# Optimization experiments

Hardware: AMD Instinct MI355X
Metric: run time of the kernel (lower is better)

## Reference

```python
import jax, jax.numpy as jnp
import numpy as np

LATENT = 256
SELEN = 64
MSIZE = 8
BS = 32
T = 2048
TOUCH_IN = 3
GAZE_IN = 4


def setup_inputs() -> dict:
    key = jax.random.key(0)
    ks = jax.random.split(key, 16)
    kH = 1.0 / np.sqrt(LATENT)

    def u(k, shape):
        return jax.random.uniform(k, shape, jnp.float32, -kH, kH)

    return {
        "touch_d": jax.random.normal(ks[0], (BS, T, TOUCH_IN), jnp.float32),
        "gaze_d": jax.random.normal(ks[1], (BS, T, GAZE_IN), jnp.float32),
        # scale so start + SELEN <= T always (avoids the random fallback branch)
        "l": jax.random.uniform(ks[2], (BS, MSIZE), jnp.float32) * ((T - SELEN) / T),
        "tW_ih": u(ks[3], (4 * LATENT, TOUCH_IN)),
        "tW_hh": u(ks[4], (4 * LATENT, LATENT)),
        "tb_ih": u(ks[5], (4 * LATENT,)),
        "tb_hh": u(ks[6], (4 * LATENT,)),
        "gW_ih": u(ks[7], (4 * LATENT, GAZE_IN)),
        "gW_hh": u(ks[8], (4 * LATENT, LATENT)),
        "gb_ih": u(ks[9], (4 * LATENT,)),
        "gb_hh": u(ks[10], (4 * LATENT,)),
        "t_lin_w": u(ks[11], (LATENT, LATENT)),
        "t_lin_b": u(ks[12], (LATENT,)),
        "g_lin_w": u(ks[13], (LATENT, LATENT)),
        "g_lin_b": u(ks[14], (LATENT,)),
    }


def lstm(x, W_ih, W_hh, b_ih, b_hh):
    # x: [B, T, D] -> outputs [B, T, H]; PyTorch gate order i, f, g, o
    B = x.shape[0]
    H = W_hh.shape[1]
    x_proj = x @ W_ih.T + (b_ih + b_hh)  # [B, T, 4H] precomputed input GEMM

    def step(carry, xt):
        h, c = carry
        gates = xt + h @ W_hh.T
        i, f, g, o = jnp.split(gates, 4, axis=-1)
        c = jax.nn.sigmoid(f) * c + jax.nn.sigmoid(i) * jnp.tanh(g)
        h = jax.nn.sigmoid(o) * jnp.tanh(c)
        return (h, c), h

    h0 = jnp.zeros((B, H), x.dtype)
    _, ys = jax.lax.scan(step, (h0, h0), jnp.swapaxes(x_proj, 0, 1))
    return jnp.swapaxes(ys, 0, 1)


def glimpse_mean(emb, starts):
    # emb: [B, T, H]; starts: [B, M] int window starts; mean over M windows of SELEN
    idx = (starts[:, :, None] + jnp.arange(SELEN)).reshape(emb.shape[0], MSIZE * SELEN)
    gathered = jnp.take_along_axis(emb, idx[..., None], axis=1)  # [B, M*SELEN, H]
    return gathered.mean(axis=1)


def reference(touch_d, gaze_d, l, tW_ih, tW_hh, tb_ih, tb_hh,
              gW_ih, gW_hh, gb_ih, gb_hh, t_lin_w, t_lin_b, g_lin_w, g_lin_b):
    touch_out = lstm(touch_d, tW_ih, tW_hh, tb_ih, tb_hh)
    gaze_out = lstm(gaze_d, gW_ih, gW_hh, gb_ih, gb_hh)
    touch_emb = jax.nn.relu(touch_out) @ t_lin_w.T + t_lin_b  # [B, T, H]
    gaze_emb = jax.nn.relu(gaze_out) @ g_lin_w.T + g_lin_b

    touch_mean = touch_emb.mean(axis=1)
    gaze_mean = gaze_emb.mean(axis=1)

    starts = (l * T).astype(jnp.int32)  # [B, M], guaranteed start + SELEN <= T
    touch_attn = glimpse_mean(touch_emb, starts)
    gaze_attn = glimpse_mean(gaze_emb, starts)

    return jnp.concatenate([touch_mean, touch_attn, gaze_mean, gaze_attn], axis=-1)
```

## Files before the change

### kernel.cpp

```cpp
#include <hip/hip_runtime.h>

#define HDIM 256
#define TLEN 2048
#define SELEN 64
#define MSZ 8

typedef _Float16 f16x2 __attribute__((ext_vector_type(2)));
typedef unsigned int u32x16 __attribute__((ext_vector_type(16)));

__device__ __forceinline__ float dot2f(unsigned int w, unsigned int h, float acc) {
  return __builtin_amdgcn_fdot2(__builtin_bit_cast(f16x2, w),
                                __builtin_bit_cast(f16x2, h), acc, false);
}

__device__ __forceinline__ unsigned int pack2(float a, float b) {
  f16x2 v;
  v.x = (_Float16)a; v.y = (_Float16)b;
  return __builtin_bit_cast(unsigned int, v);
}

__device__ __forceinline__ float sigm(float x)   { return 1.0f / (1.0f + __expf(-x)); }
__device__ __forceinline__ float tanh_f(float x) { return 1.0f - 2.0f / (__expf(2.0f * x) + 1.0f); }

#define WO_OFF    0
#define WIH_OFF   131072
#define CNT_OFF   147456
#define H2_OFF    149504
#define LDS_BYTES 150528

extern __shared__ unsigned char smem[];

#define LOADG16(V, RP, B) do {                                                  \
    float2 a0 = (RP)[(B)+0],  a1 = (RP)[(B)+1],  a2 = (RP)[(B)+2],  a3 = (RP)[(B)+3];   \
    float2 a4 = (RP)[(B)+4],  a5 = (RP)[(B)+5],  a6 = (RP)[(B)+6],  a7 = (RP)[(B)+7];   \
    float2 a8 = (RP)[(B)+8],  a9 = (RP)[(B)+9],  aA = (RP)[(B)+10], aB = (RP)[(B)+11];  \
    float2 aC = (RP)[(B)+12], aD = (RP)[(B)+13], aE = (RP)[(B)+14], aF = (RP)[(B)+15];  \
    V[0]  = pack2(a0.x, a0.y); V[1]  = pack2(a1.x, a1.y);                       \
    V[2]  = pack2(a2.x, a2.y); V[3]  = pack2(a3.x, a3.y);                       \
    V[4]  = pack2(a4.x, a4.y); V[5]  = pack2(a5.x, a5.y);                       \
    V[6]  = pack2(a6.x, a6.y); V[7]  = pack2(a7.x, a7.y);                       \
    V[8]  = pack2(a8.x, a8.y); V[9]  = pack2(a9.x, a9.y);                       \
    V[10] = pack2(aA.x, aA.y); V[11] = pack2(aB.x, aB.y);                       \
    V[12] = pack2(aC.x, aC.y); V[13] = pack2(aD.x, aD.y);                       \
    V[14] = pack2(aE.x, aE.y); V[15] = pack2(aF.x, aF.y);                       \
    __builtin_amdgcn_sched_barrier(0);                                          \
  } while (0)

#define JBLK(WIv, WFv, WGv, Q, HC, OC, PF, JN)                                  \
  { const uint4 hh = HC, wo = OC;                                               \
    if (PF) { HC = hv4[JN]; OC = wo4r[(JN) * 512]; }                            \
    ai = dot2f(WIv[4*(Q)+0], hh.x, ai); af = dot2f(WFv[4*(Q)+0], hh.x, af);     \
    ag = dot2f(WGv[4*(Q)+0], hh.x, ag); ao = dot2f(wo.x,         hh.x, ao);     \
    ai = dot2f(WIv[4*(Q)+1], hh.y, ai); af = dot2f(WFv[4*(Q)+1], hh.y, af);     \
    ag = dot2f(WGv[4*(Q)+1], hh.y, ag); ao = dot2f(wo.y,         hh.y, ao);     \
    ai = dot2f(WIv[4*(Q)+2], hh.z, ai); af = dot2f(WFv[4*(Q)+2], hh.z, af);     \
    ag = dot2f(WGv[4*(Q)+2], hh.z, ag); ao = dot2f(wo.z,         hh.z, ao);     \
    ai = dot2f(WIv[4*(Q)+3], hh.w, ai); af = dot2f(WFv[4*(Q)+3], hh.w, af);     \
    ag = dot2f(WGv[4*(Q)+3], hh.w, ag); ao = dot2f(wo.w,         hh.w, ao);     \
    __builtin_amdgcn_sched_barrier(0); }

__global__ void
__attribute__((amdgpu_flat_work_group_size(512, 512),
               amdgpu_waves_per_eu(2, 2),
               amdgpu_num_vgpr(256)))
lstm_seq_kernel(const float* __restrict__ touch, const float* __restrict__ gaze,
                const float* __restrict__ l,
                const float* __restrict__ tWih, const float* __restrict__ tWhh,
                const float* __restrict__ tbih, const float* __restrict__ tbhh,
                const float* __restrict__ gWih, const float* __restrict__ gWhh,
                const float* __restrict__ gbih, const float* __restrict__ gbhh,
                float* __restrict__ ws)
{
  const int bid  = (int)blockIdx.x;
  const int lsel = bid >> 5;
  const int b    = bid & 31;
  const int tid  = (int)threadIdx.x;
  const int lane = tid & 63;
  const int wv   = tid >> 6;
  const int n    = wv * 32 + (lane & 31);
  const int kh   = lane >> 5;
  const int c0   = kh * 128;

  const float* __restrict__ x   = lsel ? gaze : touch;
  const float* __restrict__ Wih = lsel ? gWih : tWih;
  const float* __restrict__ Whh = lsel ? gWhh : tWhh;
  const float* __restrict__ bih = lsel ? gbih : tbih;
  const float* __restrict__ bhh = lsel ? gbhh : tbhh;
  const int D = lsel ? 4 : 3;

  unsigned int*  woL  = (unsigned int*)(smem + WO_OFF);
  float4*        wihF = (float4*)(smem + WIH_OFF);
  unsigned char* cntL = smem + CNT_OFF;

  u32x16 wi0, wi1, wi2, wi3, wf0, wf1, wf2, wf3, wg0, wg1, wg2, wg3;
  {
    const float2* ri = (const float2*)(Whh + (size_t)n * HDIM + c0);
    const float2* rf = (const float2*)(Whh + (size_t)(n + 256) * HDIM + c0);
    const float2* rg = (const float2*)(Whh + (size_t)(n + 512) * HDIM + c0);
    LOADG16(wi0, ri, 0);  LOADG16(wi1, ri, 16);  LOADG16(wi2, ri, 32);  LOADG16(wi3, ri, 48);
    LOADG16(wf0, rf, 0);  LOADG16(wf1, rf, 16);  LOADG16(wf2, rf, 32);  LOADG16(wf3, rf, 48);
    LOADG16(wg0, rg, 0);  LOADG16(wg1, rg, 16);  LOADG16(wg2, rg, 32);  LOADG16(wg3, rg, 48);
  }
  {
    const float2* ro = (const float2*)(Whh + (size_t)(n + 768) * HDIM + c0);
    uint4* wo4 = (uint4*)woL;
    #pragma unroll
    for (int jb = 0; jb < 4; ++jb) {
      #pragma unroll
      for (int q = 0; q < 4; ++q) {
        const int j = jb * 4 + q;
        float2 e0 = ro[4*j], e1 = ro[4*j+1], e2 = ro[4*j+2], e3 = ro[4*j+3];
        uint4 v;
        v.x = pack2(e0.x, e0.y); v.y = pack2(e1.x, e1.y);
        v.z = pack2(e2.x, e2.y); v.w = pack2(e3.x, e3.y);
        wo4[j * 512 + tid] = v;
      }
      __builtin_amdgcn_sched_barrier(0);
    }
  }

  for (int r = tid; r < 1024; r += 512) {
    const float* wr = Wih + (size_t)r * D;
    float4 v;
    v.x = wr[0]; v.y = wr[1]; v.z = wr[2];
    v.w = (D == 4) ? wr[3] : 0.0f;
    wihF[r] = v;
  }
  __builtin_amdgcn_sched_barrier(0);

  {
    int s0 = (int)(l[b * MSZ + 0] * 2048.0f), s1 = (int)(l[b * MSZ + 1] * 2048.0f);
    int s2 = (int)(l[b * MSZ + 2] * 2048.0f), s3 = (int)(l[b * MSZ + 3] * 2048.0f);
    int s4 = (int)(l[b * MSZ + 4] * 2048.0f), s5 = (int)(l[b * MSZ + 5] * 2048.0f);
    int s6 = (int)(l[b * MSZ + 6] * 2048.0f), s7 = (int)(l[b * MSZ + 7] * 2048.0f);
    for (int t0 = tid; t0 < TLEN; t0 += 512) {
      int c = 0;
      c += (t0 >= s0 && t0 < s0 + SELEN) ? 1 : 0;
      c += (t0 >= s1 && t0 < s1 + SELEN) ? 1 : 0;
      c += (t0 >= s2 && t0 < s2 + SELEN) ? 1 : 0;
      c += (t0 >= s3 && t0 < s3 + SELEN) ? 1 : 0;
      c += (t0 >= s4 && t0 < s4 + SELEN) ? 1 : 0;
      c += (t0 >= s5 && t0 < s5 + SELEN) ? 1 : 0;
      c += (t0 >= s6 && t0 < s6 + SELEN) ? 1 : 0;
      c += (t0 >= s7 && t0 < s7 + SELEN) ? 1 : 0;
      cntL[t0] = (unsigned char)c;
    }
  }

  if (tid < 128) ((unsigned int*)(smem + H2_OFF))[tid] = 0u;

  const float bi_ = bih[n]       + bhh[n];
  const float bf_ = bih[n + 256] + bhh[n + 256];
  const float bg_ = bih[n + 512] + bhh[n + 512];
  const float bo_ = bih[n + 768] + bhh[n + 768];

  float cst = 0.f, Sall = 0.f, Swin = 0.f;
  const float* xrow = x + (size_t)b * TLEN * D;

  float x0 = xrow[0], x1 = xrow[1], x2 = xrow[2];
  float x3 = (D == 4) ? xrow[3] : 0.0f;

  __syncthreads();

  float cw = (float)cntL[0];
  const uint4* wo4r = ((const uint4*)woL) + tid;

  for (int t = 0; t < TLEN; ++t) {
    const int tn = (t + 1 < TLEN) ? (t + 1) : t;
    const float* xp = xrow + (size_t)tn * D;
    const float nx0 = xp[0], nx1 = xp[1], nx2 = xp[2];
    const float nx3 = (D == 4) ? xp[3] : 0.0f;
    const float ncw = (float)cntL[tn];

    const uint4* hv4 = (const uint4*)(smem + H2_OFF + (t & 1) * 512 + kh * 256);

    uint4 hA = hv4[0], oA = wo4r[0];
    uint4 hB = hv4[1], oB = wo4r[512];

    float ai = 0.f, af = 0.f, ag = 0.f, ao = 0.f;
    JBLK(wi0, wf0, wg0, 0, hA, oA, 1,  2)
    JBLK(wi0, wf0, wg0, 1, hB, oB, 1,  3)
    JBLK(wi0, wf0, wg0, 2, hA, oA, 1,  4)
    JBLK(wi0, wf0, wg0, 3, hB, oB, 1,  5)
    JBLK(wi1, wf1, wg1, 0, hA, oA, 1,  6)
    JBLK(wi1, wf1, wg1, 1, hB, oB, 1,  7)
    JBLK(wi1, wf1, wg1, 2, hA, oA, 1,  8)
    JBLK(wi1, wf1, wg1, 3, hB, oB, 1,  9)
    JBLK(wi2, wf2, wg2, 0, hA, oA, 1, 10)
    JBLK(wi2, wf2, wg2, 1, hB, oB, 1, 11)
    JBLK(wi2, wf2, wg2, 2, hA, oA, 1, 12)
    JBLK(wi2, wf2, wg2, 3, hB, oB, 1, 13)
    JBLK(wi3, wf3, wg3, 0, hA, oA, 1, 14)
    JBLK(wi3, wf3, wg3, 1, hB, oB, 1, 15)
    JBLK(wi3, wf3, wg3, 2, hA, oA, 0,  0)
    JBLK(wi3, wf3, wg3, 3, hB, oB, 0,  0)

    ai += __shfl_xor(ai, 32);
    af += __shfl_xor(af, 32);
    ag += __shfl_xor(ag, 32);
    ao += __shfl_xor(ao, 32);

    const float4 wr0 = wihF[n];
    const float4 wr1 = wihF[n + 256];
    const float4 wr2 = wihF[n + 512];
    const float4 wr3 = wihF[n + 768];
    const float gi = ai + bi_ + x0*wr0.x + x1*wr0.y + x2*wr0.z + x3*wr0.w;
    const float gf = af + bf_ + x0*wr1.x + x1*wr1.y + x2*wr1.z + x3*wr1.w;
    const float gg = ag + bg_ + x0*wr2.x + x1*wr2.y + x2*wr2.z + x3*wr2.w;
    const float go = ao + bo_ + x0*wr3.x + x1*wr3.y + x2*wr3.z + x3*wr3.w;
    const float si = sigm(gi), sf = sigm(gf), so = sigm(go);
    const float tg = tanh_f(gg);
    cst = sf * cst + si * tg;
    const float hv = so * tanh_f(cst);
    const float rh = fmaxf(hv, 0.0f);
    Sall += rh;
    Swin += cw * rh;

    if (kh == 0)
      ((_Float16*)(smem + H2_OFF + ((t + 1) & 1) * 512))[n] = (_Float16)hv;

    x0 = nx0; x1 = nx1; x2 = nx2; x3 = nx3; cw = ncw;

    __syncthreads();
  }

  if (kh == 0) {
    ws[((0 * 2 + lsel) * 32 + b) * HDIM + n] = Sall;
    ws[((1 * 2 + lsel) * 32 + b) * HDIM + n] = Swin;
  }
}

__global__ void proj_kernel(const float* __restrict__ ws,
                            const float* __restrict__ tlw, const float* __restrict__ tlb,
                            const float* __restrict__ glw, const float* __restrict__ glb,
                            float* __restrict__ out)
{
  const int b    = (int)blockIdx.x >> 2;
  const int seg  = (int)blockIdx.x & 3;
  const int j    = (int)threadIdx.x;
  const int lsel = seg >> 1;
  const int kind = seg & 1;
  const float* __restrict__ W    = lsel ? glw : tlw;
  const float* __restrict__ bias = lsel ? glb : tlb;
  const float scale = kind ? (1.0f / 512.0f) : (1.0f / 2048.0f);

  __shared__ float Sv[HDIM];
  Sv[j] = ws[((kind * 2 + lsel) * 32 + b) * HDIM + j] * scale;
  __syncthreads();

  float acc = bias[j];
  const float4* wr4 = (const float4*)(W + (size_t)j * HDIM);
  #pragma unroll 8
  for (int k4 = 0; k4 < HDIM / 4; ++k4) {
    const float4 w = wr4[k4];
    acc = fmaf(Sv[4*k4],     w.x, acc);
    acc = fmaf(Sv[4*k4 + 1], w.y, acc);
    acc = fmaf(Sv[4*k4 + 2], w.z, acc);
    acc = fmaf(Sv[4*k4 + 3], w.w, acc);
  }
  out[(size_t)b * 1024 + seg * HDIM + j] = acc;
}

extern "C" void kernel_launch(void* const* d_in, const int* in_sizes, int n_in,
                              void* d_out, int out_size, void* d_ws, size_t ws_size,
                              hipStream_t stream) {
  (void)in_sizes; (void)n_in; (void)out_size; (void)ws_size;
  const float* touch = (const float*)d_in[0];
  const float* gaze  = (const float*)d_in[1];
  const float* l     = (const float*)d_in[2];
  const float* tWih  = (const float*)d_in[3];
  const float* tWhh  = (const float*)d_in[4];
  const float* tbih  = (const float*)d_in[5];
  const float* tbhh  = (const float*)d_in[6];
  const float* gWih  = (const float*)d_in[7];
  const float* gWhh  = (const float*)d_in[8];
  const float* gbih  = (const float*)d_in[9];
  const float* gbhh  = (const float*)d_in[10];
  const float* tlw   = (const float*)d_in[11];
  const float* tlb   = (const float*)d_in[12];
  const float* glw   = (const float*)d_in[13];
  const float* glb   = (const float*)d_in[14];
  float* out = (float*)d_out;
  float* ws  = (float*)d_ws;

  hipFuncSetAttribute(reinterpret_cast<const void*>(&lstm_seq_kernel),
                      hipFuncAttributeMaxDynamicSharedMemorySize, LDS_BYTES);

  hipLaunchKernelGGL(lstm_seq_kernel, dim3(64), dim3(512), LDS_BYTES, stream,
                     touch, gaze, l, tWih, tWhh, tbih, tbhh,
                     gWih, gWhh, gbih, gbhh, ws);
  hipLaunchKernelGGL(proj_kernel, dim3(128), dim3(256), 0, stream,
                     ws, tlw, tlb, glw, glb, out);
}
```

Measured before the change: 3.510 ms.

## Split each hidden unit across four lanes with 1024-thread blocks

Doubles the block to 1024 threads and splits each hidden unit's 256-wide recurrent dot product across four lanes of 64 elements instead of two lanes of 128. This halves the register-resident weights and the serial dot work per thread on the per-step critical path, at the cost of a two-level shuffle reduction and a barrier across 16 waves. The h buffer is padded per 64-unit group to reduce LDS bank conflicts, and the summed biases move into LDS. The x prefetch into the next step is dropped in favour of wave-uniform loads via readfirstlane, which puts a global load back on each step and tightens register pressure to about 128 VGPRs per thread.

```diff
diff --git a/kernel.cpp b/kernel.cpp
--- a/kernel.cpp
+++ b/kernel.cpp
@@ -19,14 +19,19 @@
   return __builtin_bit_cast(unsigned int, v);
 }
 
+__device__ __forceinline__ float uni(float v) {
+  return __builtin_bit_cast(float, __builtin_amdgcn_readfirstlane(__builtin_bit_cast(int, v)));
+}
+
 __device__ __forceinline__ float sigm(float x)   { return 1.0f / (1.0f + __expf(-x)); }
 __device__ __forceinline__ float tanh_f(float x) { return 1.0f - 2.0f / (__expf(2.0f * x) + 1.0f); }
 
 #define WO_OFF    0
 #define WIH_OFF   131072
-#define CNT_OFF   147456
-#define H2_OFF    149504
-#define LDS_BYTES 150528
+#define BIAS_OFF  147456
+#define CNT_OFF   151552
+#define H2_OFF    153600
+#define LDS_BYTES 154752
 
 extern __shared__ unsigned char smem[];
 
@@ -48,7 +53,7 @@
 
 #define JBLK(WIv, WFv, WGv, Q, HC, OC, PF, JN)                                  \
   { const uint4 hh = HC, wo = OC;                                               \
-    if (PF) { HC = hv4[JN]; OC = wo4r[(JN) * 512]; }                            \
+    if (PF) { HC = hq[JN]; OC = wo4r[(JN) * 1024]; }                            \
     ai = dot2f(WIv[4*(Q)+0], hh.x, ai); af = dot2f(WFv[4*(Q)+0], hh.x, af);     \
     ag = dot2f(WGv[4*(Q)+0], hh.x, ag); ao = dot2f(wo.x,         hh.x, ao);     \
     ai = dot2f(WIv[4*(Q)+1], hh.y, ai); af = dot2f(WFv[4*(Q)+1], hh.y, af);     \
@@ -59,17 +64,14 @@
     ag = dot2f(WGv[4*(Q)+3], hh.w, ag); ao = dot2f(wo.w,         hh.w, ao);     \
     __builtin_amdgcn_sched_barrier(0); }
 
-__global__ void
-__attribute__((amdgpu_flat_work_group_size(512, 512),
-               amdgpu_waves_per_eu(2, 2),
-               amdgpu_num_vgpr(256)))
-lstm_seq_kernel(const float* __restrict__ touch, const float* __restrict__ gaze,
-                const float* __restrict__ l,
-                const float* __restrict__ tWih, const float* __restrict__ tWhh,
-                const float* __restrict__ tbih, const float* __restrict__ tbhh,
-                const float* __restrict__ gWih, const float* __restrict__ gWhh,
-                const float* __restrict__ gbih, const float* __restrict__ gbhh,
-                float* __restrict__ ws)
+__global__ __launch_bounds__(1024)
+void lstm_seq_kernel(const float* __restrict__ touch, const float* __restrict__ gaze,
+                     const float* __restrict__ l,
+                     const float* __restrict__ tWih, const float* __restrict__ tWhh,
+                     const float* __restrict__ tbih, const float* __restrict__ tbhh,
+                     const float* __restrict__ gWih, const float* __restrict__ gWhh,
+                     const float* __restrict__ gbih, const float* __restrict__ gbhh,
+                     float* __restrict__ ws)
 {
   const int bid  = (int)blockIdx.x;
   const int lsel = bid >> 5;
@@ -77,9 +79,9 @@
   const int tid  = (int)threadIdx.x;
   const int lane = tid & 63;
   const int wv   = tid >> 6;
-  const int n    = wv * 32 + (lane & 31);
-  const int kh   = lane >> 5;
-  const int c0   = kh * 128;
+  const int n    = wv * 16 + (lane >> 2);
+  const int kq   = lane & 3;
+  const int c0   = kq * 64;
 
   const float* __restrict__ x   = lsel ? gaze : touch;
   const float* __restrict__ Wih = lsel ? gWih : tWih;
@@ -88,43 +90,47 @@
   const float* __restrict__ bhh = lsel ? gbhh : tbhh;
   const int D = lsel ? 4 : 3;
 
-  unsigned int*  woL  = (unsigned int*)(smem + WO_OFF);
+  uint4*         wo4  = (uint4*)(smem + WO_OFF);
   float4*        wihF = (float4*)(smem + WIH_OFF);
+  float4*        biasF= (float4*)(smem + BIAS_OFF);
   unsigned char* cntL = smem + CNT_OFF;
 
-  u32x16 wi0, wi1, wi2, wi3, wf0, wf1, wf2, wf3, wg0, wg1, wg2, wg3;
+  u32x16 wi0, wi1, wf0, wf1, wg0, wg1;
   {
     const float2* ri = (const float2*)(Whh + (size_t)n * HDIM + c0);
     const float2* rf = (const float2*)(Whh + (size_t)(n + 256) * HDIM + c0);
     const float2* rg = (const float2*)(Whh + (size_t)(n + 512) * HDIM + c0);
-    LOADG16(wi0, ri, 0);  LOADG16(wi1, ri, 16);  LOADG16(wi2, ri, 32);  LOADG16(wi3, ri, 48);
-    LOADG16(wf0, rf, 0);  LOADG16(wf1, rf, 16);  LOADG16(wf2, rf, 32);  LOADG16(wf3, rf, 48);
-    LOADG16(wg0, rg, 0);  LOADG16(wg1, rg, 16);  LOADG16(wg2, rg, 32);  LOADG16(wg3, rg, 48);
+    LOADG16(wi0, ri, 0);  LOADG16(wi1, ri, 16);
+    LOADG16(wf0, rf, 0);  LOADG16(wf1, rf, 16);
+    LOADG16(wg0, rg, 0);  LOADG16(wg1, rg, 16);
   }
   {
     const float2* ro = (const float2*)(Whh + (size_t)(n + 768) * HDIM + c0);
-    uint4* wo4 = (uint4*)woL;
     #pragma unroll
-    for (int jb = 0; jb < 4; ++jb) {
-      #pragma unroll
-      for (int q = 0; q < 4; ++q) {
-        const int j = jb * 4 + q;
-        float2 e0 = ro[4*j], e1 = ro[4*j+1], e2 = ro[4*j+2], e3 = ro[4*j+3];
-        uint4 v;
-        v.x = pack2(e0.x, e0.y); v.y = pack2(e1.x, e1.y);
-        v.z = pack2(e2.x, e2.y); v.w = pack2(e3.x, e3.y);
-        wo4[j * 512 + tid] = v;
-      }
-      __builtin_amdgcn_sched_barrier(0);
+    for (int j = 0; j < 8; ++j) {
+      float2 e0 = ro[4*j], e1 = ro[4*j+1], e2 = ro[4*j+2], e3 = ro[4*j+3];
+      uint4 v;
+      v.x = pack2(e0.x, e0.y); v.y = pack2(e1.x, e1.y);
+      v.z = pack2(e2.x, e2.y); v.w = pack2(e3.x, e3.y);
+      wo4[j * 1024 + tid] = v;
+      if ((j & 3) == 3) __builtin_amdgcn_sched_barrier(0);
     }
   }
 
-  for (int r = tid; r < 1024; r += 512) {
-    const float* wr = Wih + (size_t)r * D;
+  {
+    const float* wr = Wih + (size_t)tid * D;
     float4 v;
     v.x = wr[0]; v.y = wr[1]; v.z = wr[2];
     v.w = (D == 4) ? wr[3] : 0.0f;
-    wihF[r] = v;
+    wihF[tid] = v;
+  }
+  if (tid < 256) {
+    float4 v;
+    v.x = bih[tid]       + bhh[tid];
+    v.y = bih[tid + 256] + bhh[tid + 256];
+    v.z = bih[tid + 512] + bhh[tid + 512];
+    v.w = bih[tid + 768] + bhh[tid + 768];
+    biasF[tid] = v;
   }
   __builtin_amdgcn_sched_barrier(0);
 
@@ -133,7 +139,7 @@
     int s2 = (int)(l[b * MSZ + 2] * 2048.0f), s3 = (int)(l[b * MSZ + 3] * 2048.0f);
     int s4 = (int)(l[b * MSZ + 4] * 2048.0f), s5 = (int)(l[b * MSZ + 5] * 2048.0f);
     int s6 = (int)(l[b * MSZ + 6] * 2048.0f), s7 = (int)(l[b * MSZ + 7] * 2048.0f);
-    for (int t0 = tid; t0 < TLEN; t0 += 512) {
+    for (int t0 = tid; t0 < TLEN; t0 += 1024) {
       int c = 0;
       c += (t0 >= s0 && t0 < s0 + SELEN) ? 1 : 0;
       c += (t0 >= s1 && t0 < s1 + SELEN) ? 1 : 0;
@@ -147,67 +153,53 @@
     }
   }
 
-  if (tid < 128) ((unsigned int*)(smem + H2_OFF))[tid] = 0u;
-
-  const float bi_ = bih[n]       + bhh[n];
-  const float bf_ = bih[n + 256] + bhh[n + 256];
-  const float bg_ = bih[n + 512] + bhh[n + 512];
-  const float bo_ = bih[n + 768] + bhh[n + 768];
+  if (tid < 144) ((unsigned int*)(smem + H2_OFF))[tid] = 0u;
 
   float cst = 0.f, Sall = 0.f, Swin = 0.f;
   const float* xrow = x + (size_t)b * TLEN * D;
 
-  float x0 = xrow[0], x1 = xrow[1], x2 = xrow[2];
-  float x3 = (D == 4) ? xrow[3] : 0.0f;
-
   __syncthreads();
 
-  float cw = (float)cntL[0];
-  const uint4* wo4r = ((const uint4*)woL) + tid;
+  const uint4* wo4r = wo4 + tid;
+  const int hwr_base = (n >> 6) * 144 + (n & 63) * 2;
 
   for (int t = 0; t < TLEN; ++t) {
-    const int tn = (t + 1 < TLEN) ? (t + 1) : t;
-    const float* xp = xrow + (size_t)tn * D;
-    const float nx0 = xp[0], nx1 = xp[1], nx2 = xp[2];
-    const float nx3 = (D == 4) ? xp[3] : 0.0f;
-    const float ncw = (float)cntL[tn];
-
-    const uint4* hv4 = (const uint4*)(smem + H2_OFF + (t & 1) * 512 + kh * 256);
-
-    uint4 hA = hv4[0], oA = wo4r[0];
-    uint4 hB = hv4[1], oB = wo4r[512];
+    const float* xp = xrow + (size_t)t * D;
+    const float x0 = uni(xp[0]), x1 = uni(xp[1]), x2 = uni(xp[2]);
+    const float x3 = (D == 4) ? uni(xp[3]) : 0.0f;
+    const float cw = (float)cntL[t];
+
+    const uint4* hq = (const uint4*)(smem + H2_OFF + (t & 1) * 576 + kq * 144);
+
+    uint4 hA = hq[0], oA = wo4r[0];
+    uint4 hB = hq[1], oB = wo4r[1024];
 
     float ai = 0.f, af = 0.f, ag = 0.f, ao = 0.f;
-    JBLK(wi0, wf0, wg0, 0, hA, oA, 1,  2)
-    JBLK(wi0, wf0, wg0, 1, hB, oB, 1,  3)
-    JBLK(wi0, wf0, wg0, 2, hA, oA, 1,  4)
-    JBLK(wi0, wf0, wg0, 3, hB, oB, 1,  5)
-    JBLK(wi1, wf1, wg1, 0, hA, oA, 1,  6)
-    JBLK(wi1, wf1, wg1, 1, hB, oB, 1,  7)
-    JBLK(wi1, wf1, wg1, 2, hA, oA, 1,  8)
-    JBLK(wi1, wf1, wg1, 3, hB, oB, 1,  9)
-    JBLK(wi2, wf2, wg2, 0, hA, oA, 1, 10)
-    JBLK(wi2, wf2, wg2, 1, hB, oB, 1, 11)
-    JBLK(wi2, wf2, wg2, 2, hA, oA, 1, 12)
-    JBLK(wi2, wf2, wg2, 3, hB, oB, 1, 13)
-    JBLK(wi3, wf3, wg3, 0, hA, oA, 1, 14)
-    JBLK(wi3, wf3, wg3, 1, hB, oB, 1, 15)
-    JBLK(wi3, wf3, wg3, 2, hA, oA, 0,  0)
-    JBLK(wi3, wf3, wg3, 3, hB, oB, 0,  0)
-
-    ai += __shfl_xor(ai, 32);
-    af += __shfl_xor(af, 32);
-    ag += __shfl_xor(ag, 32);
-    ao += __shfl_xor(ao, 32);
+    JBLK(wi0, wf0, wg0, 0, hA, oA, 1, 2)
+    JBLK(wi0, wf0, wg0, 1, hB, oB, 1, 3)
+    JBLK(wi0, wf0, wg0, 2, hA, oA, 1, 4)
+    JBLK(wi0, wf0, wg0, 3, hB, oB, 1, 5)
+    JBLK(wi1, wf1, wg1, 0, hA, oA, 1, 6)
+    JBLK(wi1, wf1, wg1, 1, hB, oB, 1, 7)
+    JBLK(wi1, wf1, wg1, 2, hA, oA, 0, 0)
+    JBLK(wi1, wf1, wg1, 3, hB, oB, 0, 0)
+
+    ai += __shfl_xor(ai, 1); ai += __shfl_xor(ai, 2);
+    af += __shfl_xor(af, 1); af += __shfl_xor(af, 2);
+    ag += __shfl_xor(ag, 1); ag += __shfl_xor(ag, 2);
+    ao += __shfl_xor(ao, 1); ao += __shfl_xor(ao, 2);
+
+    __builtin_amdgcn_sched_barrier(0);
 
     const float4 wr0 = wihF[n];
     const float4 wr1 = wihF[n + 256];
     const float4 wr2 = wihF[n + 512];
     const float4 wr3 = wihF[n + 768];
-    const float gi = ai + bi_ + x0*wr0.x + x1*wr0.y + x2*wr0.z + x3*wr0.w;
-    const float gf = af + bf_ + x0*wr1.x + x1*wr1.y + x2*wr1.z + x3*wr1.w;
-    const float gg = ag + bg_ + x0*wr2.x + x1*wr2.y + x2*wr2.z + x3*wr2.w;
-    const float go = ao + bo_ + x0*wr3.x + x1*wr3.y + x2*wr3.z + x3*wr3.w;
+    const float4 bb  = biasF[n];
+    const float gi = ai + bb.x + x0*wr0.x + x1*wr0.y + x2*wr0.z + x3*wr0.w;
+    const float gf = af + bb.y + x0*wr1.x + x1*wr1.y + x2*wr1.z + x3*wr1.w;
+    const float gg = ag + bb.z + x0*wr2.x + x1*wr2.y + x2*wr2.z + x3*wr2.w;
+    const float go = ao + bb.w + x0*wr3.x + x1*wr3.y + x2*wr3.z + x3*wr3.w;
     const float si = sigm(gi), sf = sigm(gf), so = sigm(go);
     const float tg = tanh_f(gg);
     cst = sf * cst + si * tg;
@@ -216,15 +208,13 @@
     Sall += rh;
     Swin += cw * rh;
 
-    if (kh == 0)
-      ((_Float16*)(smem + H2_OFF + ((t + 1) & 1) * 512))[n] = (_Float16)hv;
-
-    x0 = nx0; x1 = nx1; x2 = nx2; x3 = nx3; cw = ncw;
+    if (kq == 0)
+      *(_Float16*)(smem + H2_OFF + ((t + 1) & 1) * 576 + hwr_base) = (_Float16)hv;
 
     __syncthreads();
   }
 
-  if (kh == 0) {
+  if (kq == 0) {
     ws[((0 * 2 + lsel) * 32 + b) * HDIM + n] = Sall;
     ws[((1 * 2 + lsel) * 32 + b) * HDIM + n] = Swin;
   }
@@ -286,7 +276,7 @@
   hipFuncSetAttribute(reinterpret_cast<const void*>(&lstm_seq_kernel),
                       hipFuncAttributeMaxDynamicSharedMemorySize, LDS_BYTES);
 
-  hipLaunchKernelGGL(lstm_seq_kernel, dim3(64), dim3(512), LDS_BYTES, stream,
+  hipLaunchKernelGGL(lstm_seq_kernel, dim3(64), dim3(1024), LDS_BYTES, stream,
                      touch, gaze, l, tWih, tWhh, tbih, tbhh,
                      gWih, gWhh, gbih, gbhh, ws);
   hipLaunchKernelGGL(proj_kernel, dim3(128), dim3(256), 0, stream,
```

Measured after the change: 5.349 ms. 52.4% more time.
